# Kernel optimization log

Measured on AMD Instinct MI355X. Metric: run time of the kernel, lower is better.

The kernel has to match this reference:

```python
import jax, jax.numpy as jnp
import numpy as np

D_MODEL = 1024
N_HEADS = 16
D_HEAD = D_MODEL // N_HEADS
N_INS = 3
RANK = 16
EPS = 1e-5


def gelu1p(x):
    # gelu1p feature map: 1 + GELU(x) (positive-ish feature map for linear attention)
    return 1.0 + jax.nn.gelu(x, approximate=False)


def setup_inputs() -> dict:
    key = jax.random.key(0)
    ks = jax.random.split(key, 16)
    B, T = 4, 8192
    x = jax.random.normal(ks[0], (B, T, D_MODEL), dtype=jnp.float32)
    pad_mask = jnp.ones((B, T), dtype=bool)
    s = 1.0 / np.sqrt(D_MODEL)
    wq = jax.random.normal(ks[1], (D_MODEL, D_MODEL), jnp.float32) * s
    wk = jax.random.normal(ks[2], (D_MODEL, D_MODEL), jnp.float32) * s
    wv = jax.random.normal(ks[3], (D_MODEL, D_MODEL), jnp.float32) * s
    wo = jax.random.normal(ks[4], (D_MODEL, D_MODEL), jnp.float32) * s
    sr = 1.0 / np.sqrt(RANK)
    # LoRA weights stacked over insertion points: down (n_ins, rank, d), up (n_ins, d, rank)
    # NOTE: original zero-inits 'up'; we use small random values so LoRA path is exercised.
    def lora(k1, k2):
        return (jax.random.normal(k1, (N_INS, RANK, D_MODEL), jnp.float32) * s,
                jax.random.normal(k2, (N_INS, D_MODEL, RANK), jnp.float32) * sr * 0.01)
    lqd, lqu = lora(ks[5], ks[6])
    lkd, lku = lora(ks[7], ks[8])
    lvd, lvu = lora(ks[9], ks[10])
    lod, lou = lora(ks[11], ks[12])
    return {"x": x, "pad_mask": pad_mask, "insertion_idx": 1,
            "wq": wq, "wk": wk, "wv": wv, "wo": wo,
            "lqd": lqd, "lqu": lqu, "lkd": lkd, "lku": lku,
            "lvd": lvd, "lvu": lvu, "lod": lod, "lou": lou}


def _proj(x, w, down, up):
    # base linear (no bias) + LoRA: x @ w.T + (x @ down.T) @ up.T
    return x @ w.T + (x @ down.T) @ up.T


def reference(x, pad_mask, insertion_idx, wq, wk, wv, wo,
              lqd, lqu, lkd, lku, lvd, lvu, lod, lou):
    B, T, D = x.shape
    i = insertion_idx
    q = _proj(x, wq, lqd[i], lqu[i])
    k = _proj(x, wk, lkd[i], lku[i])
    v = _proj(x, wv, lvd[i], lvu[i])
    # (B, T, H, dh) -> (B, H, T, dh)
    q = q.reshape(B, T, N_HEADS, D_HEAD).transpose(0, 2, 1, 3)
    k = k.reshape(B, T, N_HEADS, D_HEAD).transpose(0, 2, 1, 3)
    v = v.reshape(B, T, N_HEADS, D_HEAD).transpose(0, 2, 1, 3)
    q = gelu1p(q)
    k = gelu1p(k)
    m = pad_mask[:, None, :, None].astype(k.dtype)  # (B,1,T,1)
    k = k * m
    v = v * m
    context = jnp.einsum('bhtd,bhte->bhde', k, v)  # (B,H,dh,dh)
    z = k.sum(axis=-2)                              # (B,H,dh)
    num = jnp.einsum('bhtd,bhde->bhte', q, context)
    den = jnp.einsum('bhtd,bhd->bht', q, z)
    out = num / (den[..., None] + EPS)
    out = out.transpose(0, 2, 1, 3).reshape(B, T, D)
    out = _proj(out, wo, lod[i], lou[i])
    return out
```

## Files before the change

kernel.cpp:

```cpp
#include <hip/hip_runtime.h>
#include <hip/hip_bf16.h>

typedef unsigned short u16;
typedef __attribute__((ext_vector_type(8))) short short8;
typedef __attribute__((ext_vector_type(4))) float f32x4;
typedef __attribute__((ext_vector_type(4))) unsigned short us4;
typedef __attribute__((ext_vector_type(8))) unsigned short us8;

__device__ __forceinline__ u16 f2bf(float f) {
  unsigned int u = __float_as_uint(f);
  u += 0x7fffu + ((u >> 16) & 1u);
  return (u16)(u >> 16);
}
__device__ __forceinline__ float bf2f(u16 h) {
  return __uint_as_float(((unsigned int)h) << 16);
}
__device__ __forceinline__ float gelu1p_f(float x) {
  const float z  = x * 0.7071067811865475f;
  const float az = __builtin_fabsf(z);
  const float t  = __builtin_amdgcn_rcpf(__builtin_fmaf(0.3275911f, az, 1.0f));
  float pl = __builtin_fmaf(1.061405429f, t, -1.453152027f);
  pl = __builtin_fmaf(pl, t, 1.421413741f);
  pl = __builtin_fmaf(pl, t, -0.284496736f);
  pl = __builtin_fmaf(pl, t, 0.254829592f);
  pl = pl * t;
  const float e = __builtin_amdgcn_exp2f(-az * az * 1.4426950408889634f);
  float erfa = __builtin_fmaf(-pl, e, 1.0f);
  erfa = __builtin_copysignf(erfa, z);
  return __builtin_fmaf(x, 0.5f * (1.0f + erfa), 1.0f);
}
__device__ __forceinline__ void gll16(const void* g, void* l) {
  __builtin_amdgcn_global_load_lds(
      (const __attribute__((address_space(1))) unsigned int*)g,
      (__attribute__((address_space(3))) unsigned int*)l, 16, 0, 0);
}
#define FENCE() __builtin_amdgcn_sched_barrier(0)
#define BARRIER() __builtin_amdgcn_s_barrier()
#define LGKM0() do { asm volatile("s_waitcnt lgkmcnt(0)" ::: "memory"); FENCE(); } while (0)
#define VMCNT4() do { asm volatile("s_waitcnt vmcnt(4)" ::: "memory"); FENCE(); } while (0)
#define MFMA16(a, b, c) __builtin_amdgcn_mfma_f32_16x16x32_bf16(a, b, c, 0, 0, 0)

__global__ __launch_bounds__(256)
void build_weff(const float* __restrict__ wq, const float* __restrict__ wk,
                const float* __restrict__ wv, const float* __restrict__ wo,
                const float* __restrict__ lqd, const float* __restrict__ lqu,
                const float* __restrict__ lkd, const float* __restrict__ lku,
                const float* __restrict__ lvd, const float* __restrict__ lvu,
                const float* __restrict__ lod, const float* __restrict__ lou,
                const int* __restrict__ idxp,
                u16* __restrict__ wqkv, u16* __restrict__ wout) {
  const int blk = blockIdx.x;
  const int p = blk >> 10;
  const int n = blk & 1023;
  const int i = *idxp;
  const float* W  = (p == 0) ? wq  : (p == 1) ? wk  : (p == 2) ? wv  : wo;
  const float* Dn = ((p == 0) ? lqd : (p == 1) ? lkd : (p == 2) ? lvd : lod) + (size_t)i * 16 * 1024;
  const float* Up = ((p == 0) ? lqu : (p == 1) ? lku : (p == 2) ? lvu : lou) + (size_t)i * 1024 * 16;

  float up[16];
#pragma unroll
  for (int r = 0; r < 16; ++r) up[r] = Up[n * 16 + r];

  const int k0 = threadIdx.x << 2;
  f32x4 acc = *(const f32x4*)&W[(size_t)n * 1024 + k0];
#pragma unroll
  for (int r = 0; r < 16; ++r) {
    const f32x4 d = *(const f32x4*)&Dn[r * 1024 + k0];
#pragma unroll
    for (int j = 0; j < 4; ++j) acc[j] = __builtin_fmaf(up[r], d[j], acc[j]);
  }
  us4 o;
#pragma unroll
  for (int j = 0; j < 4; ++j) o[j] = f2bf(acc[j]);
  if (p < 3) *(us4*)&wqkv[(size_t)(p * 1024 + n) * 1024 + k0] = o;
  else       *(us4*)&wout[(size_t)n * 1024 + k0] = o;
}

__global__ void xcast(const float* __restrict__ x, u16* __restrict__ xb) {
  const size_t i = ((size_t)blockIdx.x * 256 + threadIdx.x) * 8;
  f32x4 a = *(const f32x4*)(x + i);
  f32x4 b = *(const f32x4*)(x + i + 4);
  us8 o;
#pragma unroll
  for (int j = 0; j < 4; ++j) { o[j] = f2bf(a[j]); o[j + 4] = f2bf(b[j]); }
  *(us8*)(xb + i) = o;
}

template <int MODE>
__global__ __launch_bounds__(512, 2)
void gemm8p(const u16* __restrict__ A, const u16* __restrict__ Bw,
            u16* __restrict__ qb, u16* __restrict__ kbuf, u16* __restrict__ vbuf,
            float* __restrict__ outf, const int* __restrict__ mask, int nbx) {
  const int nwg = gridDim.x;
  const int cpx = nwg >> 3;
  const int wg0 = blockIdx.x;
  const int swz = (wg0 & 7) * cpx + (wg0 >> 3);
  const int bx = swz % nbx;
  const int by = swz / nbx;
  const int row0 = by << 8, col0 = bx << 8;
  const int tid = threadIdx.x, lane = tid & 63, w = tid >> 6;
  const int wr = w >> 2, wc = w & 3;

  __shared__ __align__(16) u16 lds[2][2][2][8192];

  const int srow = (w << 4) + (lane & 15);
  const int scol = (lane >> 4) << 3;
  const u16* pA = A  + (size_t)(row0 + srow) * 1024 + scol;
  const u16* pB = Bw + (size_t)(col0 + srow) * 1024 + scol;

  auto stA = [&](int bb, int h, int ts) {
    const u16* s = pA + h * 131072 + ts * 64;
    u16* d = &lds[bb][0][h][((w << 7) + lane) << 3];
    gll16(s, d); gll16(s + 32, d + 512);
  };
  auto stB = [&](int bb, int h, int ts) {
    const u16* s = pB + h * 131072 + ts * 64;
    u16* d = &lds[bb][1][h][((w << 7) + lane) << 3];
    gll16(s, d); gll16(s + 32, d + 512);
  };
  auto LDA = [&](int bb, int m, int kk) {
    return *(const short8*)&lds[bb][0][wr][((((m << 1) | kk) << 6) | lane) << 3];
  };
  auto LDB = [&](int bb, int n, int kk) {
    const int nn = ((wc & 1) << 2) | n;
    return *(const short8*)&lds[bb][1][wc >> 1][((((nn << 1) | kk) << 6) | lane) << 3];
  };

  f32x4 acc[8][4] = {};
  short8 af[4][2], bfv[4][2];

  stA(0, 0, 0); stB(0, 0, 0); stA(0, 1, 0); stB(0, 1, 0);
  stB(1, 0, 1); stA(1, 0, 1);
  VMCNT4();
  BARRIER();

  auto tile = [&](int BUF, int t) {
    const int t1 = (t + 1 < 16) ? t + 1 : 15;
    const int t2 = (t + 2 < 16) ? t + 2 : 15;
#pragma unroll
    for (int m = 0; m < 4; ++m) { af[m][0] = LDA(BUF, m, 0); af[m][1] = LDA(BUF, m, 1); }
#pragma unroll
    for (int n = 0; n < 2; ++n) { bfv[n][0] = LDB(BUF, n, 0); bfv[n][1] = LDB(BUF, n, 1); }
    stA(BUF ^ 1, 1, t1);
    FENCE(); BARRIER(); LGKM0();
    __builtin_amdgcn_s_setprio(1);
#pragma unroll
    for (int m = 0; m < 4; ++m)
#pragma unroll
      for (int n = 0; n < 2; ++n) {
        acc[m][n] = MFMA16(af[m][0], bfv[n][0], acc[m][n]);
        acc[m][n] = MFMA16(af[m][1], bfv[n][1], acc[m][n]);
      }
    __builtin_amdgcn_s_setprio(0);
    FENCE(); BARRIER();
#pragma unroll
    for (int n = 2; n < 4; ++n) { bfv[n][0] = LDB(BUF, n, 0); bfv[n][1] = LDB(BUF, n, 1); }
    stB(BUF ^ 1, 1, t1);
    FENCE(); BARRIER(); LGKM0();
    __builtin_amdgcn_s_setprio(1);
#pragma unroll
    for (int m = 0; m < 4; ++m)
#pragma unroll
      for (int n = 2; n < 4; ++n) {
        acc[m][n] = MFMA16(af[m][0], bfv[n][0], acc[m][n]);
        acc[m][n] = MFMA16(af[m][1], bfv[n][1], acc[m][n]);
      }
    __builtin_amdgcn_s_setprio(0);
    FENCE(); BARRIER();
#pragma unroll
    for (int m = 0; m < 4; ++m) { af[m][0] = LDA(BUF, 4 + m, 0); af[m][1] = LDA(BUF, 4 + m, 1); }
    stB(BUF, 0, t2);
    FENCE(); BARRIER(); LGKM0();
    __builtin_amdgcn_s_setprio(1);
#pragma unroll
    for (int m = 0; m < 4; ++m)
#pragma unroll
      for (int n = 2; n < 4; ++n) {
        acc[4 + m][n] = MFMA16(af[m][0], bfv[n][0], acc[4 + m][n]);
        acc[4 + m][n] = MFMA16(af[m][1], bfv[n][1], acc[4 + m][n]);
      }
    __builtin_amdgcn_s_setprio(0);
    FENCE(); BARRIER();
    stA(BUF, 0, t2);
    FENCE(); BARRIER();
    __builtin_amdgcn_s_setprio(1);
#pragma unroll
    for (int m = 0; m < 4; ++m)
#pragma unroll
      for (int n = 0; n < 2; ++n) {
        acc[4 + m][n] = MFMA16(af[m][0], bfv[n][0], acc[4 + m][n]);
        acc[4 + m][n] = MFMA16(af[m][1], bfv[n][1], acc[4 + m][n]);
      }
    __builtin_amdgcn_s_setprio(0);
    FENCE();
    VMCNT4();
    BARRIER();
  };

  for (int t = 0; t < 16; t += 2) { tile(0, t); tile(1, t + 1); }

  if (MODE == 0) {
    const int cw = col0 + (wc << 6);
    const int p = cw >> 10;
    u16* dst = (p == 0) ? qb : (p == 1) ? kbuf : vbuf;
    const int cc0 = (cw & 1023) + (lane & 15);
#pragma unroll
    for (int m = 0; m < 8; ++m) {
      const int r0 = row0 + (wr << 7) + (m << 4) + ((lane >> 4) << 2);
#pragma unroll
      for (int j = 0; j < 4; ++j) {
        const int r = r0 + j;
        const float mv = (p == 0) ? 1.0f : ((mask[r] != 0) ? 1.0f : 0.0f);
#pragma unroll
        for (int n = 0; n < 4; ++n) {
          float v = acc[m][n][j];
          v = (p == 2) ? v * mv : gelu1p_f(v) * mv;
          dst[(size_t)r * 1024 + cc0 + (n << 4)] = f2bf(v);
        }
      }
    }
  } else {
    const int c0 = col0 + (wc << 6) + (lane & 15);
#pragma unroll
    for (int m = 0; m < 8; ++m) {
      const int r0 = row0 + (wr << 7) + (m << 4) + ((lane >> 4) << 2);
#pragma unroll
      for (int n = 0; n < 4; ++n)
#pragma unroll
        for (int j = 0; j < 4; ++j)
          outf[(size_t)(r0 + j) * 1024 + c0 + (n << 4)] = acc[m][n][j];
    }
  }
}

__global__ __launch_bounds__(256)
void ctx_partial(const u16* __restrict__ kbuf, const u16* __restrict__ vbuf,
                 float* __restrict__ Cpart, float* __restrict__ zpart) {
  const int tid = threadIdx.x;
  const int bh = blockIdx.y, chunk = blockIdx.x;
  const int b = bh >> 4, h = bh & 15;
  const size_t rowbase = (size_t)b * 8192 + (size_t)chunk * 1024;
  const int colbase = h * 64;

  __shared__ __align__(16) u16 ktl[64][64];
  __shared__ __align__(16) u16 vtl[64][64];

  const int d0 = (tid >> 4) << 2;
  const int e0 = (tid & 15) << 2;
  const int ei0 = (tid & 15) == 0;

  float acc[4][4] = {};
  float zacc[4] = {};

  const int lr = tid >> 3;
  const int lc = (tid & 7) << 3;

  for (int tile = 0; tile < 16; ++tile) {
    const size_t gr = rowbase + tile * 64;
#pragma unroll
    for (int half = 0; half < 2; ++half) {
      const int rr = lr + half * 32;
      const size_t off = (gr + rr) * 1024 + colbase + lc;
      *(us8*)&ktl[rr][lc] = *(const us8*)&kbuf[off];
      *(us8*)&vtl[rr][lc] = *(const us8*)&vbuf[off];
    }
    __syncthreads();
    for (int t = 0; t < 64; ++t) {
      us4 ku = *(const us4*)&ktl[t][d0];
      us4 vu = *(const us4*)&vtl[t][e0];
      float kf[4], vf[4];
#pragma unroll
      for (int j = 0; j < 4; ++j) { kf[j] = bf2f(ku[j]); vf[j] = bf2f(vu[j]); }
#pragma unroll
      for (int j = 0; j < 4; ++j)
#pragma unroll
        for (int i = 0; i < 4; ++i) acc[j][i] += kf[j] * vf[i];
      if (ei0) {
#pragma unroll
        for (int j = 0; j < 4; ++j) zacc[j] += kf[j];
      }
    }
    __syncthreads();
  }
  float* cp = Cpart + (size_t)(bh * 8 + chunk) * 4096;
#pragma unroll
  for (int j = 0; j < 4; ++j)
#pragma unroll
    for (int i = 0; i < 4; ++i) cp[(d0 + j) * 64 + e0 + i] = acc[j][i];
  if (ei0) {
    float* zp = zpart + (size_t)(bh * 8 + chunk) * 64;
#pragma unroll
    for (int j = 0; j < 4; ++j) zp[d0 + j] = zacc[j];
  }
}

__global__ void ctx_reduce(const float* __restrict__ Cpart, const float* __restrict__ zpart,
                           u16* __restrict__ Cb) {
  const int bh = blockIdx.x, tid = threadIdx.x;
  for (int idx = tid; idx < 5120; idx += 256) {
    const int d = idx / 80;
    const int e = idx - d * 80;
    float s = 0.f;
    if (e < 64) {
#pragma unroll
      for (int c = 0; c < 8; ++c) s += Cpart[(size_t)(bh * 8 + c) * 4096 + d * 64 + e];
    } else if (e == 64) {
#pragma unroll
      for (int c = 0; c < 8; ++c) s += zpart[(size_t)(bh * 8 + c) * 64 + d];
    }
    Cb[(size_t)bh * 5120 + idx] = f2bf(s);
  }
}

__global__ __launch_bounds__(256)
void attn_out(const u16* __restrict__ qbuf, const u16* __restrict__ Cb,
              u16* __restrict__ ratio) {
  const int tid = threadIdx.x, lane = tid & 63, wave = tid >> 6;
  const int bh = blockIdx.y, b = bh >> 4, h = bh & 15;
  const int t0 = blockIdx.x * 256 + wave * 64;
  const size_t mbase = (size_t)b * 8192;
  const u16* cb = Cb + (size_t)bh * 5120;

  short8 bfrag[5][2];
#pragma unroll
  for (int nt = 0; nt < 5; ++nt)
#pragma unroll
    for (int kf = 0; kf < 2; ++kf) {
      short8 f;
#pragma unroll
      for (int j = 0; j < 8; ++j) {
        const int d = kf * 32 + ((lane >> 4) << 3) + j;
        f[j] = (short)cb[d * 80 + nt * 16 + (lane & 15)];
      }
      bfrag[nt][kf] = f;
    }

  f32x4 acc[4][5] = {};
#pragma unroll
  for (int mt = 0; mt < 4; ++mt) {
    const int tr = t0 + mt * 16 + (lane & 15);
    const u16* qrow = qbuf + (mbase + tr) * 1024 + h * 64 + ((lane >> 4) << 3);
    short8 a0 = *(const short8*)qrow;
    short8 a1 = *(const short8*)(qrow + 32);
#pragma unroll
    for (int nt = 0; nt < 5; ++nt) {
      acc[mt][nt] = MFMA16(a0, bfrag[nt][0], acc[mt][nt]);
      acc[mt][nt] = MFMA16(a1, bfrag[nt][1], acc[mt][nt]);
    }
  }

#pragma unroll
  for (int mt = 0; mt < 4; ++mt) {
#pragma unroll
    for (int j = 0; j < 4; ++j) {
      const float den = __shfl(acc[mt][4][j], lane & 48, 64);
      const float inv = 1.0f / (den + 1e-5f);
      const int tr = t0 + mt * 16 + ((lane >> 4) << 2) + j;
      u16* orow = ratio + (mbase + tr) * 1024 + h * 64;
#pragma unroll
      for (int nt = 0; nt < 4; ++nt)
        orow[nt * 16 + (lane & 15)] = f2bf(acc[mt][nt][j] * inv);
    }
  }
}

extern "C" void kernel_launch(void* const* d_in, const int* in_sizes, int n_in,
                              void* d_out, int out_size, void* d_ws, size_t ws_size,
                              hipStream_t stream) {
  (void)in_sizes; (void)n_in; (void)out_size; (void)ws_size;
  const float* x = (const float*)d_in[0];
  const int* mask = (const int*)d_in[1];
  const int* idx = (const int*)d_in[2];
  const float* wq = (const float*)d_in[3];
  const float* wk = (const float*)d_in[4];
  const float* wv = (const float*)d_in[5];
  const float* wo = (const float*)d_in[6];
  const float* lqd = (const float*)d_in[7];
  const float* lqu = (const float*)d_in[8];
  const float* lkd = (const float*)d_in[9];
  const float* lku = (const float*)d_in[10];
  const float* lvd = (const float*)d_in[11];
  const float* lvu = (const float*)d_in[12];
  const float* lod = (const float*)d_in[13];
  const float* lou = (const float*)d_in[14];
  float* out = (float*)d_out;

  char* ws = (char*)d_ws;
  u16* xb    = (u16*)ws;
  u16* wqkv  = (u16*)(ws + (64ll << 20));
  u16* wo_b  = (u16*)(ws + (70ll << 20));
  u16* qb    = (u16*)(ws + (72ll << 20));
  u16* kb    = (u16*)(ws + (136ll << 20));
  u16* vb    = (u16*)(ws + (200ll << 20));
  float* Cpart = (float*)(ws + (264ll << 20));
  float* zpart = (float*)(ws + (272ll << 20));
  u16* Cb    = (u16*)(ws + (273ll << 20));
  u16* ratio = xb;

  build_weff<<<dim3(4096), dim3(256), 0, stream>>>(wq, wk, wv, wo,
      lqd, lqu, lkd, lku, lvd, lvu, lod, lou, idx, wqkv, wo_b);
  xcast<<<dim3(16384), dim3(256), 0, stream>>>(x, xb);
  gemm8p<0><<<dim3(1536), dim3(512), 0, stream>>>(xb, wqkv, qb, kb, vb, nullptr, mask, 12);
  ctx_partial<<<dim3(8, 64), dim3(256), 0, stream>>>(kb, vb, Cpart, zpart);
  ctx_reduce<<<dim3(64), dim3(256), 0, stream>>>(Cpart, zpart, Cb);
  attn_out<<<dim3(32, 64), dim3(256), 0, stream>>>(qb, Cb, ratio);
  gemm8p<1><<<dim3(512), dim3(512), 0, stream>>>(ratio, wo_b, nullptr, nullptr, nullptr, out, mask, 4);
}
```

Before: 551.0 us.

## Compute K^T V context with MFMA instead of scalar FMA loop

```diff
diff --git a/kernel.cpp b/kernel.cpp
--- a/kernel.cpp
+++ b/kernel.cpp
@@ -197,7 +197,8 @@
     BARRIER();
   };
 
-  for (int t = 0; t < 16; t += 2) { tile(0, t); tile(1, t + 1); }
+#pragma unroll
+  for (int it = 0; it < 8; ++it) { tile(0, 2 * it); tile(1, 2 * it + 1); }
 
   if (MODE == 0) {
     const int cw = col0 + (wc << 6);
@@ -233,64 +234,60 @@
   }
 }
 
-__global__ __launch_bounds__(256)
-void ctx_partial(const u16* __restrict__ kbuf, const u16* __restrict__ vbuf,
-                 float* __restrict__ Cpart, float* __restrict__ zpart) {
-  const int tid = threadIdx.x;
-  const int bh = blockIdx.y, chunk = blockIdx.x;
+__global__ __launch_bounds__(64)
+void ctx_mfma(const u16* __restrict__ kbuf, const u16* __restrict__ vbuf,
+              float* __restrict__ Cpart, float* __restrict__ zpart) {
+  const int lane = threadIdx.x;
+  const int bh = blockIdx.y, sl = blockIdx.x;
   const int b = bh >> 4, h = bh & 15;
-  const size_t rowbase = (size_t)b * 8192 + (size_t)chunk * 1024;
-  const int colbase = h * 64;
-
-  __shared__ __align__(16) u16 ktl[64][64];
-  __shared__ __align__(16) u16 vtl[64][64];
-
-  const int d0 = (tid >> 4) << 2;
-  const int e0 = (tid & 15) << 2;
-  const int ei0 = (tid & 15) == 0;
-
-  float acc[4][4] = {};
-  float zacc[4] = {};
-
-  const int lr = tid >> 3;
-  const int lc = (tid & 7) << 3;
-
-  for (int tile = 0; tile < 16; ++tile) {
-    const size_t gr = rowbase + tile * 64;
-#pragma unroll
-    for (int half = 0; half < 2; ++half) {
-      const int rr = lr + half * 32;
-      const size_t off = (gr + rr) * 1024 + colbase + lc;
-      *(us8*)&ktl[rr][lc] = *(const us8*)&kbuf[off];
-      *(us8*)&vtl[rr][lc] = *(const us8*)&vbuf[off];
-    }
-    __syncthreads();
-    for (int t = 0; t < 64; ++t) {
-      us4 ku = *(const us4*)&ktl[t][d0];
-      us4 vu = *(const us4*)&vtl[t][e0];
-      float kf[4], vf[4];
-#pragma unroll
-      for (int j = 0; j < 4; ++j) { kf[j] = bf2f(ku[j]); vf[j] = bf2f(vu[j]); }
-#pragma unroll
-      for (int j = 0; j < 4; ++j)
-#pragma unroll
-        for (int i = 0; i < 4; ++i) acc[j][i] += kf[j] * vf[i];
-      if (ei0) {
-#pragma unroll
-        for (int j = 0; j < 4; ++j) zacc[j] += kf[j];
-      }
-    }
-    __syncthreads();
-  }
-  float* cp = Cpart + (size_t)(bh * 8 + chunk) * 4096;
-#pragma unroll
-  for (int j = 0; j < 4; ++j)
-#pragma unroll
-    for (int i = 0; i < 4; ++i) cp[(d0 + j) * 64 + e0 + i] = acc[j][i];
-  if (ei0) {
-    float* zp = zpart + (size_t)(bh * 8 + chunk) * 64;
-#pragma unroll
-    for (int j = 0; j < 4; ++j) zp[d0 + j] = zacc[j];
+  const size_t base = ((size_t)b * 8192 + (size_t)sl * 512) * 1024 + h * 64;
+  const int colA = lane & 15;
+  const int tj0 = (lane >> 4) << 3;
+
+  short8 ones;
+#pragma unroll
+  for (int j = 0; j < 8; ++j) ones[j] = (short)0x3F80;
+
+  f32x4 acc[4][5] = {};
+
+  for (int c = 0; c < 16; ++c) {
+    const size_t tbase = base + (size_t)(c * 32 + tj0) * 1024;
+    short8 af[4], bv[4];
+#pragma unroll
+    for (int s = 0; s < 4; ++s) {
+      const u16* pk = kbuf + tbase + s * 16 + colA;
+      const u16* pv = vbuf + tbase + s * 16 + colA;
+      short8 a, v;
+#pragma unroll
+      for (int j = 0; j < 8; ++j) { a[j] = (short)pk[j * 1024]; v[j] = (short)pv[j * 1024]; }
+      af[s] = a; bv[s] = v;
+    }
+#pragma unroll
+    for (int di = 0; di < 4; ++di) {
+#pragma unroll
+      for (int ei = 0; ei < 4; ++ei)
+        acc[di][ei] = MFMA16(af[di], bv[ei], acc[di][ei]);
+      acc[di][4] = MFMA16(af[di], ones, acc[di][4]);
+    }
+  }
+
+  float* cp = Cpart + (size_t)(bh * 16 + sl) * 4096;
+  const int el = lane & 15, rb = (lane >> 4) << 2;
+#pragma unroll
+  for (int di = 0; di < 4; ++di)
+#pragma unroll
+    for (int j = 0; j < 4; ++j) {
+      const int d = di * 16 + rb + j;
+#pragma unroll
+      for (int ei = 0; ei < 4; ++ei)
+        cp[d * 64 + ei * 16 + el] = acc[di][ei][j];
+    }
+  if (el == 0) {
+    float* zp = zpart + (size_t)(bh * 16 + sl) * 64;
+#pragma unroll
+    for (int di = 0; di < 4; ++di)
+#pragma unroll
+      for (int j = 0; j < 4; ++j) zp[di * 16 + rb + j] = acc[di][4][j];
   }
 }
 
@@ -303,10 +300,10 @@
     float s = 0.f;
     if (e < 64) {
 #pragma unroll
-      for (int c = 0; c < 8; ++c) s += Cpart[(size_t)(bh * 8 + c) * 4096 + d * 64 + e];
+      for (int c = 0; c < 16; ++c) s += Cpart[(size_t)(bh * 16 + c) * 4096 + d * 64 + e];
     } else if (e == 64) {
 #pragma unroll
-      for (int c = 0; c < 8; ++c) s += zpart[(size_t)(bh * 8 + c) * 64 + d];
+      for (int c = 0; c < 16; ++c) s += zpart[(size_t)(bh * 16 + c) * 64 + d];
     }
     Cb[(size_t)bh * 5120 + idx] = f2bf(s);
   }
@@ -392,7 +389,7 @@
   u16* qb    = (u16*)(ws + (72ll << 20));
   u16* kb    = (u16*)(ws + (136ll << 20));
   u16* vb    = (u16*)(ws + (200ll << 20));
-  float* Cpart = (float*)(ws + (264ll << 20));
+  float* Cpart = (float*)ws;
   float* zpart = (float*)(ws + (272ll << 20));
   u16* Cb    = (u16*)(ws + (273ll << 20));
   u16* ratio = xb;
@@ -401,7 +398,7 @@
       lqd, lqu, lkd, lku, lvd, lvu, lod, lou, idx, wqkv, wo_b);
   xcast<<<dim3(16384), dim3(256), 0, stream>>>(x, xb);
   gemm8p<0><<<dim3(1536), dim3(512), 0, stream>>>(xb, wqkv, qb, kb, vb, nullptr, mask, 12);
-  ctx_partial<<<dim3(8, 64), dim3(256), 0, stream>>>(kb, vb, Cpart, zpart);
+  ctx_mfma<<<dim3(16, 64), dim3(64), 0, stream>>>(kb, vb, Cpart, zpart);
   ctx_reduce<<<dim3(64), dim3(256), 0, stream>>>(Cpart, zpart, Cb);
   attn_out<<<dim3(32, 64), dim3(256), 0, stream>>>(qb, Cb, ratio);
   gemm8p<1><<<dim3(512), dim3(512), 0, stream>>>(ratio, wo_b, nullptr, nullptr, nullptr, out, mask, 4);
```

Result: faster. 491.1 us (-10.9%).
